# Optimization experiments

Hardware: AMD Instinct MI355X
Metric: run time of the kernel (lower is better)

## Reference

```python
import jax, jax.numpy as jnp
import numpy as np

BETA = 5.5
ALPHA = 0.5

def _l2norm(x, eps=1e-12):
    # matches torch F.normalize(dim=-1): x / max(||x||, eps)
    n = jnp.sqrt(jnp.sum(x * x, axis=-1, keepdims=True))
    return x / jnp.maximum(n, eps)

def setup_inputs() -> dict:
    key = jax.random.key(0)
    k1, k2 = jax.random.split(key)
    query_features = jax.random.normal(k1, (4096, 512), dtype=jnp.float32)
    support_keys = jax.random.normal(k2, (16384, 512), dtype=jnp.float32)
    return {"query_features": query_features, "support_keys": support_keys}

def reference(query_features, support_keys):
    cache_keys = _l2norm(support_keys)              # (N, D)
    q = _l2norm(query_features)                     # (B, D)
    affinity = jnp.einsum('bd,nd->bn', q, cache_keys)   # (B, N) cosine sims
    affinity = jnp.exp(-BETA * (1.0 - affinity))
    retrieved = jnp.einsum('bn,nd->bd', affinity, cache_keys)  # (B, D)
    return query_features + ALPHA * retrieved
```

## Files before the change

### kernel.cpp

```cpp
#include <hip/hip_runtime.h>
#include <cstdint>
#include <cstddef>

#define BETA 5.5f
#define ALPHA 0.5f

constexpr int D   = 512;
constexpr int NB  = 4096;
constexpr int NK  = 16384;
constexpr int BQ  = 64;
constexpr int BN  = 64;
constexpr int NSPLIT = 4;
constexpr int NRANGE = NK / NSPLIT;
constexpr int CHUNKS = NRANGE / BN;
constexpr int KROW = D + 8;
constexpr int PROW = BN + 8;

typedef __attribute__((ext_vector_type(8)))  short    short8;
typedef __attribute__((ext_vector_type(4)))  float    floatx4;
typedef __attribute__((ext_vector_type(4)))  uint32_t uint4v;
typedef __attribute__((ext_vector_type(2)))  uint32_t uint2v;

__device__ inline uint32_t f2bf1(float f) {
  union { float f; uint32_t u; } v; v.f = f;
  return (v.u + 0x7FFFu + ((v.u >> 16) & 1u)) >> 16;
}
__device__ inline uint32_t pack2(float a, float b) {
  return f2bf1(a) | (f2bf1(b) << 16);
}

__device__ inline void load_lds16(const void* g, void* l) {
  __builtin_amdgcn_global_load_lds(
      (const __attribute__((address_space(1))) uint32_t*)g,
      (__attribute__((address_space(3))) uint32_t*)l, 16, 0, 0);
}

__global__ void norm_q_kernel(const float* __restrict__ q,
                              float* __restrict__ out,
                              unsigned short* __restrict__ Qn) {
  const int wave = threadIdx.x >> 6, lane = threadIdx.x & 63;
  const int row = blockIdx.x * 4 + wave;
  const float4* qr = (const float4*)(q + (size_t)row * D);
  float4 a = qr[lane * 2];
  float4 b = qr[lane * 2 + 1];
  float ss = a.x*a.x + a.y*a.y + a.z*a.z + a.w*a.w
           + b.x*b.x + b.y*b.y + b.z*b.z + b.w*b.w;
#pragma unroll
  for (int m = 32; m >= 1; m >>= 1) ss += __shfl_xor(ss, m, 64);
  const float sc = 1.0f / fmaxf(sqrtf(ss), 1e-12f);
  float4* orow = (float4*)(out + (size_t)row * D);
  orow[lane * 2]     = a;
  orow[lane * 2 + 1] = b;
  uint4v w;
  w.x = pack2(a.x*sc, a.y*sc); w.y = pack2(a.z*sc, a.w*sc);
  w.z = pack2(b.x*sc, b.y*sc); w.w = pack2(b.z*sc, b.w*sc);
  *(uint4v*)(Qn + (size_t)row * D + lane * 8) = w;
}

__global__ void norm_k_kernel(const float* __restrict__ k,
                              unsigned short* __restrict__ Kn,
                              unsigned short* __restrict__ KnT) {
  __shared__ unsigned short tile[64 * KROW];
  const int wave = threadIdx.x >> 6, lane = threadIdx.x & 63;
  const int n0 = blockIdx.x * 64;
#pragma unroll
  for (int i = 0; i < 4; ++i) {
    const int rl = wave * 4 + i;
    const int n  = n0 + rl;
    const float4* kr = (const float4*)(k + (size_t)n * D);
    float4 a = kr[lane * 2], b = kr[lane * 2 + 1];
    float ss = a.x*a.x + a.y*a.y + a.z*a.z + a.w*a.w
             + b.x*b.x + b.y*b.y + b.z*b.z + b.w*b.w;
#pragma unroll
    for (int m = 32; m >= 1; m >>= 1) ss += __shfl_xor(ss, m, 64);
    const float sc = 1.0f / fmaxf(sqrtf(ss), 1e-12f);
    uint4v w;
    w.x = pack2(a.x*sc, a.y*sc); w.y = pack2(a.z*sc, a.w*sc);
    w.z = pack2(b.x*sc, b.y*sc); w.w = pack2(b.z*sc, b.w*sc);
    *(uint4v*)(Kn + (size_t)n * D + lane * 8) = w;
    *(uint4v*)&tile[rl * KROW + lane * 8]     = w;
  }
  __syncthreads();
  const int dsub = threadIdx.x >> 3;
  const int nl   = (threadIdx.x & 7) * 8;
#pragma unroll
  for (int iter = 0; iter < 4; ++iter) {
    const int d = iter * 128 + dsub;
    uint4v w;
    w.x = (uint32_t)tile[(nl+0)*KROW + d] | ((uint32_t)tile[(nl+1)*KROW + d] << 16);
    w.y = (uint32_t)tile[(nl+2)*KROW + d] | ((uint32_t)tile[(nl+3)*KROW + d] << 16);
    w.z = (uint32_t)tile[(nl+4)*KROW + d] | ((uint32_t)tile[(nl+5)*KROW + d] << 16);
    w.w = (uint32_t)tile[(nl+6)*KROW + d] | ((uint32_t)tile[(nl+7)*KROW + d] << 16);
    *(uint4v*)(KnT + (size_t)d * NK + n0 + nl) = w;
  }
}

__global__ __launch_bounds__(512, 2) void fused_kernel(
    const unsigned short* __restrict__ Qn,
    const unsigned short* __restrict__ Kn,
    const unsigned short* __restrict__ KnT,
    float* __restrict__ out) {
  __shared__ unsigned short K_lds[2][BN * KROW];
  __shared__ unsigned short P_lds[2][BQ * PROW];

  const int tid  = threadIdx.x;
  const int wave = tid >> 6, lane = tid & 63;
  const int l15  = lane & 15, quad = lane >> 4;
  const int nsplit = blockIdx.x & (NSPLIT - 1);
  const int qtile  = blockIdx.x >> 2;
  const int q0     = qtile * BQ;
  const int nbase  = nsplit * NRANGE;

  if (wave < 4) {
    const int sw = wave;
    const int qh = wave & 1, nh = wave >> 1;
    short8 qf[2][16];
    {
      const unsigned short* qrow0 = Qn + (size_t)(q0 + qh * 32 + l15) * D + quad * 8;
#pragma unroll
      for (int qt = 0; qt < 2; ++qt)
#pragma unroll
        for (int kb = 0; kb < 16; ++kb)
          qf[qt][kb] = *(const short8*)(qrow0 + (size_t)qt * 16 * D + kb * 32);
    }

    floatx4 sacc[2][2];

    auto stage = [&](int ch, int buf) {
#pragma unroll
      for (int i = 0; i < 16; ++i) {
        const int row = sw * 16 + i;
        load_lds16(Kn + (size_t)(nbase + ch * BN + row) * D + lane * 8,
                   &K_lds[buf][row * KROW]);
      }
    };
    auto a_read8 = [&](int buf, int kb0, short8* af) {
#pragma unroll
      for (int i = 0; i < 4; ++i) {
        af[2*i]   = *(const short8*)&K_lds[buf][(nh*32 +      l15) * KROW + (kb0+i)*32 + quad*8];
        af[2*i+1] = *(const short8*)&K_lds[buf][(nh*32 + 16 + l15) * KROW + (kb0+i)*32 + quad*8];
      }
    };
    auto g1c = [&](const short8* af, int kb0) {
      __builtin_amdgcn_s_setprio(1);
#pragma unroll
      for (int i = 0; i < 4; ++i) {
        sacc[0][0] = __builtin_amdgcn_mfma_f32_16x16x32_bf16(af[2*i],   qf[0][kb0+i], sacc[0][0], 0, 0, 0);
        sacc[0][1] = __builtin_amdgcn_mfma_f32_16x16x32_bf16(af[2*i],   qf[1][kb0+i], sacc[0][1], 0, 0, 0);
        sacc[1][0] = __builtin_amdgcn_mfma_f32_16x16x32_bf16(af[2*i+1], qf[0][kb0+i], sacc[1][0], 0, 0, 0);
        sacc[1][1] = __builtin_amdgcn_mfma_f32_16x16x32_bf16(af[2*i+1], qf[1][kb0+i], sacc[1][1], 0, 0, 0);
      }
      __builtin_amdgcn_s_setprio(0);
    };
    auto gemm1_region = [&](int buf) {
#pragma unroll
      for (int nt = 0; nt < 2; ++nt)
#pragma unroll
        for (int qt = 0; qt < 2; ++qt) sacc[nt][qt] = (floatx4){0.f, 0.f, 0.f, 0.f};
      short8 afA[8], afB[8];
      a_read8(buf, 0, afA);
      a_read8(buf, 4, afB);
      g1c(afA, 0);
      a_read8(buf, 8, afA);
      g1c(afB, 4);
      a_read8(buf, 12, afB);
      g1c(afA, 8);
      g1c(afB, 12);
    };
    auto exp_pw = [&](int buf) {
#pragma unroll
      for (int qt = 0; qt < 2; ++qt)
#pragma unroll
        for (int nt = 0; nt < 2; ++nt) {
          const floatx4 s = sacc[nt][qt];
          uint2v w;
          w.x = pack2(__expf(BETA * (s[0] - 1.f)), __expf(BETA * (s[1] - 1.f)));
          w.y = pack2(__expf(BETA * (s[2] - 1.f)), __expf(BETA * (s[3] - 1.f)));
          *(uint2v*)&P_lds[buf][(qh*32 + qt*16 + l15) * PROW + nh*32 + nt*16 + quad*4] = w;
        }
    };

    stage(0, 0);
    asm volatile("s_waitcnt vmcnt(0)" ::: "memory");
    asm volatile("s_barrier" ::: "memory");
    stage(1, 1);
    gemm1_region(0);
    exp_pw(0);
    asm volatile("s_waitcnt vmcnt(0) lgkmcnt(0)" ::: "memory");
    asm volatile("s_barrier" ::: "memory");

#pragma unroll 1
    for (int r = 0; r + 2 < CHUNKS; ++r) {
      stage(r + 2, r & 1);
      gemm1_region((r + 1) & 1);
      exp_pw((r + 1) & 1);
      asm volatile("s_waitcnt vmcnt(0) lgkmcnt(0)" ::: "memory");
      asm volatile("s_barrier" ::: "memory");
    }
    gemm1_region((CHUNKS - 1) & 1);
    exp_pw((CHUNKS - 1) & 1);
    asm volatile("s_waitcnt lgkmcnt(0)" ::: "memory");
    asm volatile("s_barrier" ::: "memory");
  } else {
    const int w4 = wave - 4;
    floatx4 oacc[4][8] = {};
    short8 ktf[2][8];
    const unsigned short* ktb = KnT + (size_t)(w4 * 128 + l15) * NK + nbase + quad * 8;

    auto ldKT = [&](short8* kt, int c, int kb2) {
#pragma unroll
      for (int td = 0; td < 8; ++td)
        kt[td] = *(const short8*)(ktb + (size_t)td * 16 * NK + c * BN + kb2 * 32);
    };
    auto pf_read = [&](int pbuf, int kb2, short8* pf) {
#pragma unroll
      for (int tr = 0; tr < 4; ++tr)
        pf[tr] = *(const short8*)&P_lds[pbuf][(tr*16 + l15) * PROW + kb2*32 + quad*8];
    };
    auto g2c = [&](const short8* pf, const short8* kt) {
      __builtin_amdgcn_s_setprio(1);
#pragma unroll
      for (int td = 0; td < 8; ++td)
#pragma unroll
        for (int tr = 0; tr < 4; ++tr)
          oacc[tr][td] = __builtin_amdgcn_mfma_f32_16x16x32_bf16(
              pf[tr], kt[td], oacc[tr][td], 0, 0, 0);
      __builtin_amdgcn_s_setprio(0);
    };

    ldKT(ktf[0], 0, 0); ldKT(ktf[1], 0, 1);
    asm volatile("s_barrier" ::: "memory");
    asm volatile("s_barrier" ::: "memory");

#pragma unroll 1
    for (int r = 0; r + 2 < CHUNKS; ++r) {
      short8 pf0[4], pf1[4];
      pf_read(r & 1, 0, pf0);
      pf_read(r & 1, 1, pf1);
      g2c(pf0, ktf[0]);
      ldKT(ktf[0], r + 1, 0);
      g2c(pf1, ktf[1]);
      ldKT(ktf[1], r + 1, 1);
      asm volatile("s_barrier" ::: "memory");
    }
    {
      const int r = CHUNKS - 2;
      short8 pf0[4], pf1[4];
      pf_read(r & 1, 0, pf0);
      pf_read(r & 1, 1, pf1);
      g2c(pf0, ktf[0]);
      ldKT(ktf[0], CHUNKS - 1, 0);
      g2c(pf1, ktf[1]);
      ldKT(ktf[1], CHUNKS - 1, 1);
      asm volatile("s_barrier" ::: "memory");
    }
    {
      short8 pf0[4], pf1[4];
      pf_read((CHUNKS - 1) & 1, 0, pf0);
      pf_read((CHUNKS - 1) & 1, 1, pf1);
      g2c(pf0, ktf[0]);
      g2c(pf1, ktf[1]);
    }

    const int colbase = w4 * 128 + l15;
#pragma unroll
    for (int tr = 0; tr < 4; ++tr)
#pragma unroll
      for (int td = 0; td < 8; ++td)
#pragma unroll
        for (int r4 = 0; r4 < 4; ++r4)
          atomicAdd(out + (size_t)(q0 + tr*16 + quad*4 + r4) * D + colbase + td*16,
                    ALPHA * oacc[tr][td][r4]);
  }
}

extern "C" void kernel_launch(void* const* d_in, const int* in_sizes, int n_in,
                              void* d_out, int out_size, void* d_ws, size_t ws_size,
                              hipStream_t stream) {
  (void)in_sizes; (void)n_in; (void)out_size; (void)ws_size;
  const float* q = (const float*)d_in[0];
  const float* k = (const float*)d_in[1];
  float* out = (float*)d_out;
  unsigned short* Qn  = (unsigned short*)d_ws;
  unsigned short* Kn  = Qn + (size_t)NB * D;
  unsigned short* KnT = Kn + (size_t)NK * D;

  hipLaunchKernelGGL(norm_q_kernel, dim3(NB / 4),  dim3(256),  0, stream, q, out, Qn);
  hipLaunchKernelGGL(norm_k_kernel, dim3(NK / 64), dim3(1024), 0, stream, k, Kn, KnT);
  hipLaunchKernelGGL(fused_kernel, dim3((NB / BQ) * NSPLIT), dim3(512), 0, stream,
                     Qn, Kn, KnT, out);
}
```

Before: 266.5 us.

## Replace block barriers with LDS flag counters and triple-buffer P between warp roles

Replaces the block-wide s_barrier handshakes between the producer waves (GEMM1 plus exp) and the consumer waves (GEMM2) with per-buffer LDS counters that waves spin on and bump atomically. P_lds becomes a triple buffer, so producers can run further ahead of consumers and the two roles are less tightly coupled. The aim is to remove lockstep stalls in the warp-specialized pipeline. The cost is spin-wait overhead with s_sleep and extra LDS atomics, and the hand-written waitcnt and flag logic carries a risk of memory-ordering or deadlock bugs.

```diff
diff --git a/kernel.cpp b/kernel.cpp
--- a/kernel.cpp
+++ b/kernel.cpp
@@ -33,6 +33,15 @@
   __builtin_amdgcn_global_load_lds(
       (const __attribute__((address_space(1))) uint32_t*)g,
       (__attribute__((address_space(3))) uint32_t*)l, 16, 0, 0);
+}
+
+__device__ inline void spin_ge(volatile uint32_t* f, uint32_t tgt) {
+  while (*f < tgt) __builtin_amdgcn_s_sleep(1);
+  asm volatile("" ::: "memory");
+}
+__device__ inline void bump(uint32_t* f) {
+  asm volatile("" ::: "memory");
+  if ((threadIdx.x & 63) == 0) atomicAdd(f, 1u);
 }
 
 __global__ void norm_q_kernel(const float* __restrict__ q,
@@ -101,7 +110,8 @@
     const unsigned short* __restrict__ KnT,
     float* __restrict__ out) {
   __shared__ unsigned short K_lds[2][BN * KROW];
-  __shared__ unsigned short P_lds[2][BQ * PROW];
+  __shared__ unsigned short P_lds[3][BQ * PROW];
+  __shared__ uint32_t flags[12];
 
   const int tid  = threadIdx.x;
   const int wave = tid >> 6, lane = tid & 63;
@@ -110,6 +120,14 @@
   const int qtile  = blockIdx.x >> 2;
   const int q0     = qtile * BQ;
   const int nbase  = nsplit * NRANGE;
+
+  uint32_t* kcnt  = &flags[0];
+  uint32_t* kdone = &flags[2];
+  uint32_t* pprod = &flags[4];
+  uint32_t* pcons = &flags[7];
+
+  if (tid < 12) flags[tid] = 0;
+  __syncthreads();
 
   if (wave < 4) {
     const int sw = wave;
@@ -167,7 +185,7 @@
       g1c(afA, 8);
       g1c(afB, 12);
     };
-    auto exp_pw = [&](int buf) {
+    auto exp_pw = [&](int slot) {
 #pragma unroll
       for (int qt = 0; qt < 2; ++qt)
 #pragma unroll
@@ -176,31 +194,35 @@
           uint2v w;
           w.x = pack2(__expf(BETA * (s[0] - 1.f)), __expf(BETA * (s[1] - 1.f)));
           w.y = pack2(__expf(BETA * (s[2] - 1.f)), __expf(BETA * (s[3] - 1.f)));
-          *(uint2v*)&P_lds[buf][(qh*32 + qt*16 + l15) * PROW + nh*32 + nt*16 + quad*4] = w;
+          *(uint2v*)&P_lds[slot][(qh*32 + qt*16 + l15) * PROW + nh*32 + nt*16 + quad*4] = w;
         }
     };
 
     stage(0, 0);
     asm volatile("s_waitcnt vmcnt(0)" ::: "memory");
-    asm volatile("s_barrier" ::: "memory");
+    bump(&kcnt[0]);
     stage(1, 1);
-    gemm1_region(0);
-    exp_pw(0);
-    asm volatile("s_waitcnt vmcnt(0) lgkmcnt(0)" ::: "memory");
-    asm volatile("s_barrier" ::: "memory");
 
 #pragma unroll 1
-    for (int r = 0; r + 2 < CHUNKS; ++r) {
-      stage(r + 2, r & 1);
-      gemm1_region((r + 1) & 1);
-      exp_pw((r + 1) & 1);
-      asm volatile("s_waitcnt vmcnt(0) lgkmcnt(0)" ::: "memory");
-      asm volatile("s_barrier" ::: "memory");
+    for (uint32_t p = 0; p < CHUNKS; ++p) {
+      const int buf = p & 1, slot = p % 3;
+      spin_ge(&kcnt[buf], 4 * (p >> 1) + 4);
+      gemm1_region(buf);
+      bump(&kdone[buf]);
+      if (p + 2 < CHUNKS) {
+        spin_ge(&kdone[buf], 4 * (p >> 1) + 4);
+        stage(p + 2, buf);
+        asm volatile("s_waitcnt vmcnt(16)" ::: "memory");
+        bump(&kcnt[buf ^ 1]);
+      } else if (p + 1 < CHUNKS) {
+        asm volatile("s_waitcnt vmcnt(0)" ::: "memory");
+        bump(&kcnt[buf ^ 1]);
+      }
+      spin_ge(&pcons[slot], 4 * (p / 3));
+      exp_pw(slot);
+      asm volatile("s_waitcnt lgkmcnt(0)" ::: "memory");
+      bump(&pprod[slot]);
     }
-    gemm1_region((CHUNKS - 1) & 1);
-    exp_pw((CHUNKS - 1) & 1);
-    asm volatile("s_waitcnt lgkmcnt(0)" ::: "memory");
-    asm volatile("s_barrier" ::: "memory");
   } else {
     const int w4 = wave - 4;
     floatx4 oacc[4][8] = {};
@@ -212,10 +234,10 @@
       for (int td = 0; td < 8; ++td)
         kt[td] = *(const short8*)(ktb + (size_t)td * 16 * NK + c * BN + kb2 * 32);
     };
-    auto pf_read = [&](int pbuf, int kb2, short8* pf) {
+    auto pf_read = [&](int slot, int kb2, short8* pf) {
 #pragma unroll
       for (int tr = 0; tr < 4; ++tr)
-        pf[tr] = *(const short8*)&P_lds[pbuf][(tr*16 + l15) * PROW + kb2*32 + quad*8];
+        pf[tr] = *(const short8*)&P_lds[slot][(tr*16 + l15) * PROW + kb2*32 + quad*8];
     };
     auto g2c = [&](const short8* pf, const short8* kt) {
       __builtin_amdgcn_s_setprio(1);
@@ -229,37 +251,19 @@
     };
 
     ldKT(ktf[0], 0, 0); ldKT(ktf[1], 0, 1);
-    asm volatile("s_barrier" ::: "memory");
-    asm volatile("s_barrier" ::: "memory");
 
 #pragma unroll 1
-    for (int r = 0; r + 2 < CHUNKS; ++r) {
+    for (uint32_t r = 0; r < CHUNKS; ++r) {
+      const int slot = r % 3;
+      spin_ge(&pprod[slot], 4 * (r / 3) + 4);
       short8 pf0[4], pf1[4];
-      pf_read(r & 1, 0, pf0);
-      pf_read(r & 1, 1, pf1);
+      pf_read(slot, 0, pf0);
+      pf_read(slot, 1, pf1);
       g2c(pf0, ktf[0]);
-      ldKT(ktf[0], r + 1, 0);
+      if (r + 1 < CHUNKS) ldKT(ktf[0], r + 1, 0);
       g2c(pf1, ktf[1]);
-      ldKT(ktf[1], r + 1, 1);
-      asm volatile("s_barrier" ::: "memory");
-    }
-    {
-      const int r = CHUNKS - 2;
-      short8 pf0[4], pf1[4];
-      pf_read(r & 1, 0, pf0);
-      pf_read(r & 1, 1, pf1);
-      g2c(pf0, ktf[0]);
-      ldKT(ktf[0], CHUNKS - 1, 0);
-      g2c(pf1, ktf[1]);
-      ldKT(ktf[1], CHUNKS - 1, 1);
-      asm volatile("s_barrier" ::: "memory");
-    }
-    {
-      short8 pf0[4], pf1[4];
-      pf_read((CHUNKS - 1) & 1, 0, pf0);
-      pf_read((CHUNKS - 1) & 1, 1, pf1);
-      g2c(pf0, ktf[0]);
-      g2c(pf1, ktf[1]);
+      if (r + 1 < CHUNKS) ldKT(ktf[1], r + 1, 1);
+      bump(&pcons[slot]);
     }
 
     const int colbase = w4 * 128 + l15;
```

Measured after the change: 272.2 us. +2.2%, slower.

## Move K staging to GEMM2 waves, split GEMM1 accumulators, use hardware bf16 pack

Applied to the files above, without the earlier changes.

The global-to-LDS staging of K tiles moves from the similarity (GEMM1) waves to the output (GEMM2) waves. Those waves now prefetch the next chunk alongside their transposed-K register loads, using a partial vmcnt wait, so the exp-producing waves only do MFMA and exp work. GEMM1 now alternates between two accumulator sets to break the serial MFMA dependency chain, at the cost of extra registers and one vector add. The software bf16 rounding is replaced by the v_cvt_pk_bf16_f32 instruction. The risk is that GEMM2 waves, which already carry a heavy register load, become the bottleneck.

```diff
diff --git a/kernel.cpp b/kernel.cpp
--- a/kernel.cpp
+++ b/kernel.cpp
@@ -27,6 +27,11 @@
 }
 __device__ inline uint32_t pack2(float a, float b) {
   return f2bf1(a) | (f2bf1(b) << 16);
+}
+__device__ inline uint32_t cvt_pk_bf16(float lo, float hi) {
+  uint32_t r;
+  asm("v_cvt_pk_bf16_f32 %0, %1, %2" : "=v"(r) : "v"(lo), "v"(hi));
+  return r;
 }
 
 __device__ inline void load_lds16(const void* g, void* l) {
@@ -112,7 +117,6 @@
   const int nbase  = nsplit * NRANGE;
 
   if (wave < 4) {
-    const int sw = wave;
     const int qh = wave & 1, nh = wave >> 1;
     short8 qf[2][16];
     {
@@ -124,16 +128,8 @@
           qf[qt][kb] = *(const short8*)(qrow0 + (size_t)qt * 16 * D + kb * 32);
     }
 
-    floatx4 sacc[2][2];
-
-    auto stage = [&](int ch, int buf) {
-#pragma unroll
-      for (int i = 0; i < 16; ++i) {
-        const int row = sw * 16 + i;
-        load_lds16(Kn + (size_t)(nbase + ch * BN + row) * D + lane * 8,
-                   &K_lds[buf][row * KROW]);
-      }
-    };
+    floatx4 sacc_e[2][2], sacc_o[2][2];
+
     auto a_read8 = [&](int buf, int kb0, short8* af) {
 #pragma unroll
       for (int i = 0; i < 4; ++i) {
@@ -145,10 +141,11 @@
       __builtin_amdgcn_s_setprio(1);
 #pragma unroll
       for (int i = 0; i < 4; ++i) {
-        sacc[0][0] = __builtin_amdgcn_mfma_f32_16x16x32_bf16(af[2*i],   qf[0][kb0+i], sacc[0][0], 0, 0, 0);
-        sacc[0][1] = __builtin_amdgcn_mfma_f32_16x16x32_bf16(af[2*i],   qf[1][kb0+i], sacc[0][1], 0, 0, 0);
-        sacc[1][0] = __builtin_amdgcn_mfma_f32_16x16x32_bf16(af[2*i+1], qf[0][kb0+i], sacc[1][0], 0, 0, 0);
-        sacc[1][1] = __builtin_amdgcn_mfma_f32_16x16x32_bf16(af[2*i+1], qf[1][kb0+i], sacc[1][1], 0, 0, 0);
+        auto& sa = (i & 1) ? sacc_o : sacc_e;
+        sa[0][0] = __builtin_amdgcn_mfma_f32_16x16x32_bf16(af[2*i],   qf[0][kb0+i], sa[0][0], 0, 0, 0);
+        sa[0][1] = __builtin_amdgcn_mfma_f32_16x16x32_bf16(af[2*i],   qf[1][kb0+i], sa[0][1], 0, 0, 0);
+        sa[1][0] = __builtin_amdgcn_mfma_f32_16x16x32_bf16(af[2*i+1], qf[0][kb0+i], sa[1][0], 0, 0, 0);
+        sa[1][1] = __builtin_amdgcn_mfma_f32_16x16x32_bf16(af[2*i+1], qf[1][kb0+i], sa[1][1], 0, 0, 0);
       }
       __builtin_amdgcn_s_setprio(0);
     };
@@ -156,7 +153,10 @@
 #pragma unroll
       for (int nt = 0; nt < 2; ++nt)
 #pragma unroll
-        for (int qt = 0; qt < 2; ++qt) sacc[nt][qt] = (floatx4){0.f, 0.f, 0.f, 0.f};
+        for (int qt = 0; qt < 2; ++qt) {
+          sacc_e[nt][qt] = (floatx4){0.f, 0.f, 0.f, 0.f};
+          sacc_o[nt][qt] = (floatx4){0.f, 0.f, 0.f, 0.f};
+        }
       short8 afA[8], afB[8];
       a_read8(buf, 0, afA);
       a_read8(buf, 4, afB);
@@ -167,55 +167,56 @@
       g1c(afA, 8);
       g1c(afB, 12);
     };
-    auto exp_pw = [&](int buf) {
+    auto exp_pw = [&](int slot) {
 #pragma unroll
       for (int qt = 0; qt < 2; ++qt)
 #pragma unroll
         for (int nt = 0; nt < 2; ++nt) {
-          const floatx4 s = sacc[nt][qt];
+          const floatx4 s = sacc_e[nt][qt] + sacc_o[nt][qt];
+          const float e0 = __expf(BETA * (s[0] - 1.f));
+          const float e1 = __expf(BETA * (s[1] - 1.f));
+          const float e2 = __expf(BETA * (s[2] - 1.f));
+          const float e3 = __expf(BETA * (s[3] - 1.f));
           uint2v w;
-          w.x = pack2(__expf(BETA * (s[0] - 1.f)), __expf(BETA * (s[1] - 1.f)));
-          w.y = pack2(__expf(BETA * (s[2] - 1.f)), __expf(BETA * (s[3] - 1.f)));
-          *(uint2v*)&P_lds[buf][(qh*32 + qt*16 + l15) * PROW + nh*32 + nt*16 + quad*4] = w;
+          w.x = cvt_pk_bf16(e0, e1);
+          w.y = cvt_pk_bf16(e2, e3);
+          *(uint2v*)&P_lds[slot][(qh*32 + qt*16 + l15) * PROW + nh*32 + nt*16 + quad*4] = w;
         }
     };
 
-    stage(0, 0);
     asm volatile("s_waitcnt vmcnt(0)" ::: "memory");
     asm volatile("s_barrier" ::: "memory");
-    stage(1, 1);
-    gemm1_region(0);
-    exp_pw(0);
-    asm volatile("s_waitcnt vmcnt(0) lgkmcnt(0)" ::: "memory");
-    asm volatile("s_barrier" ::: "memory");
 
 #pragma unroll 1
-    for (int r = 0; r + 2 < CHUNKS; ++r) {
-      stage(r + 2, r & 1);
-      gemm1_region((r + 1) & 1);
-      exp_pw((r + 1) & 1);
-      asm volatile("s_waitcnt vmcnt(0) lgkmcnt(0)" ::: "memory");
+    for (int r = 0; r < CHUNKS; ++r) {
+      gemm1_region(r & 1);
+      exp_pw(r & 1);
+      asm volatile("s_waitcnt lgkmcnt(0)" ::: "memory");
       asm volatile("s_barrier" ::: "memory");
     }
-    gemm1_region((CHUNKS - 1) & 1);
-    exp_pw((CHUNKS - 1) & 1);
-    asm volatile("s_waitcnt lgkmcnt(0)" ::: "memory");
-    asm volatile("s_barrier" ::: "memory");
   } else {
-    const int w4 = wave - 4;
+    const int ow = wave - 4;
     floatx4 oacc[4][8] = {};
     short8 ktf[2][8];
-    const unsigned short* ktb = KnT + (size_t)(w4 * 128 + l15) * NK + nbase + quad * 8;
-
+    const unsigned short* ktb = KnT + (size_t)(ow * 128 + l15) * NK + nbase + quad * 8;
+
+    auto stage = [&](int ch, int buf) {
+#pragma unroll
+      for (int i = 0; i < 16; ++i) {
+        const int row = ow * 16 + i;
+        load_lds16(Kn + (size_t)(nbase + ch * BN + row) * D + lane * 8,
+                   &K_lds[buf][row * KROW]);
+      }
+    };
     auto ldKT = [&](short8* kt, int c, int kb2) {
 #pragma unroll
       for (int td = 0; td < 8; ++td)
         kt[td] = *(const short8*)(ktb + (size_t)td * 16 * NK + c * BN + kb2 * 32);
     };
-    auto pf_read = [&](int pbuf, int kb2, short8* pf) {
+    auto pf_read = [&](int slot, int kb2, short8* pf) {
 #pragma unroll
       for (int tr = 0; tr < 4; ++tr)
-        pf[tr] = *(const short8*)&P_lds[pbuf][(tr*16 + l15) * PROW + kb2*32 + quad*8];
+        pf[tr] = *(const short8*)&P_lds[slot][(tr*16 + l15) * PROW + kb2*32 + quad*8];
     };
     auto g2c = [&](const short8* pf, const short8* kt) {
       __builtin_amdgcn_s_setprio(1);
@@ -228,30 +229,26 @@
       __builtin_amdgcn_s_setprio(0);
     };
 
-    ldKT(ktf[0], 0, 0); ldKT(ktf[1], 0, 1);
+    stage(0, 0);
+    asm volatile("s_waitcnt vmcnt(0)" ::: "memory");
     asm volatile("s_barrier" ::: "memory");
-    asm volatile("s_barrier" ::: "memory");
 
 #pragma unroll 1
-    for (int r = 0; r + 2 < CHUNKS; ++r) {
-      short8 pf0[4], pf1[4];
-      pf_read(r & 1, 0, pf0);
-      pf_read(r & 1, 1, pf1);
-      g2c(pf0, ktf[0]);
-      ldKT(ktf[0], r + 1, 0);
-      g2c(pf1, ktf[1]);
-      ldKT(ktf[1], r + 1, 1);
-      asm volatile("s_barrier" ::: "memory");
-    }
-    {
-      const int r = CHUNKS - 2;
-      short8 pf0[4], pf1[4];
-      pf_read(r & 1, 0, pf0);
-      pf_read(r & 1, 1, pf1);
-      g2c(pf0, ktf[0]);
-      ldKT(ktf[0], CHUNKS - 1, 0);
-      g2c(pf1, ktf[1]);
-      ldKT(ktf[1], CHUNKS - 1, 1);
+    for (int r = 0; r < CHUNKS; ++r) {
+      if (r + 1 < CHUNKS) stage(r + 1, (r + 1) & 1);
+      if (r >= 1) {
+        short8 pf0[4], pf1[4];
+        pf_read((r - 1) & 1, 0, pf0);
+        pf_read((r - 1) & 1, 1, pf1);
+        g2c(pf0, ktf[0]);
+        ldKT(ktf[0], r, 0);
+        g2c(pf1, ktf[1]);
+        ldKT(ktf[1], r, 1);
+      } else {
+        ldKT(ktf[0], 0, 0);
+        ldKT(ktf[1], 0, 1);
+      }
+      asm volatile("s_waitcnt vmcnt(16)" ::: "memory");
       asm volatile("s_barrier" ::: "memory");
     }
     {
@@ -262,7 +259,7 @@
       g2c(pf1, ktf[1]);
     }
 
-    const int colbase = w4 * 128 + l15;
+    const int colbase = ow * 128 + l15;
 #pragma unroll
     for (int tr = 0; tr < 4; ++tr)
 #pragma unroll
```

Measured after the change: 292.9 us. +9.9%, slower.
